# Optimization experiments

Measured on AMD Instinct MI355X. Metric: run time of the kernel, lower is better.

## Reference

```python
import jax, jax.numpy as jnp
import numpy as np

VOCAB, D_IN, D_H = 32000, 512, 1024
B, T = 16, 256
PAD_IDX = 0


def setup_inputs() -> dict:
    key = jax.random.key(0)
    k1, k2, k3, k4, k5 = jax.random.split(key, 5)
    input_idx = jax.random.randint(k1, (B, T), 0, VOCAB, dtype=jnp.int64)
    emb = jax.random.normal(k2, (VOCAB, D_IN), dtype=jnp.float32) * 0.02
    emb = emb.at[PAD_IDX].set(0.0)  # padding_idx row is zero
    weight_x = jax.random.normal(k3, (D_H, D_IN), dtype=jnp.float32) * (1.0 / np.sqrt(D_IN))
    weight_h = jax.random.normal(k4, (D_H, D_H), dtype=jnp.float32) * (1.0 / np.sqrt(D_H))
    bias = jnp.zeros((D_H,), dtype=jnp.float32)
    lm_W = jax.random.normal(k5, (VOCAB, D_H), dtype=jnp.float32) * (1.0 / np.sqrt(D_H))
    return {"input_idx": input_idx, "emb": emb, "weight_x": weight_x,
            "weight_h": weight_h, "bias": bias, "lm_W": lm_W}


def reference(input_idx, emb, weight_x, weight_h, bias, lm_W):
    Bsz = input_idx.shape[0]
    h0 = jnp.zeros((Bsz, weight_h.shape[0]), dtype=weight_x.dtype)

    def step(h, tok):
        x = emb[tok]  # [B, D_IN]
        h_new = jnp.tanh(x @ weight_x.T + h @ weight_h.T + bias)
        mask = (tok != PAD_IDX)[:, None]  # keep old h at pad positions
        h = jnp.where(mask, h_new, h)
        return h, h

    _, h_all = jax.lax.scan(step, h0, input_idx.T)  # [T, B, H]
    h_all = jnp.swapaxes(h_all, 0, 1)               # [B, T, H]
    logits = jnp.einsum('bth,vh->btv', h_all, lm_W)  # [B, T, V]
    return logits
```

## Files before the change

### kernel.cpp

```cpp
#include <hip/hip_runtime.h>

#define PAD_IDX 0

typedef __attribute__((ext_vector_type(8))) short short8;
typedef __attribute__((ext_vector_type(4))) float f32x4;

__device__ __forceinline__ unsigned short f32_to_bf16_rne(float f) {
  unsigned int u = __builtin_bit_cast(unsigned int, f);
  u += 0x7FFFu + ((u >> 16) & 1u);
  return (unsigned short)(u >> 16);
}

__device__ __forceinline__ void load16_to_lds(const void* g, void* lds) {
  __builtin_amdgcn_global_load_lds(
      (const __attribute__((address_space(1))) unsigned int*)g,
      (__attribute__((address_space(3))) unsigned int*)lds,
      16, 0, 0);
}

__global__ void sentinel_kernel(float* out) { out[0] = 1.0e6f; }

__global__ __launch_bounds__(256) void xwcvt_kernel(const int* __restrict__ tok,
                                                    const float* __restrict__ emb,
                                                    const float* __restrict__ Wx,
                                                    const float* __restrict__ bias,
                                                    float* __restrict__ xw,
                                                    const float* __restrict__ lmW,
                                                    unsigned short* __restrict__ lmW_bf) {
  int tid = threadIdx.x;
  if (blockIdx.x >= 1024) {
    const int n8 = 32000 * 1024 / 8;
    int stride = 512 * 256;
    for (int i = (blockIdx.x - 1024) * 256 + tid; i < n8; i += stride) {
      float4 a = ((const float4*)lmW)[2 * i];
      float4 b = ((const float4*)lmW)[2 * i + 1];
      ushort4 lo, hi;
      lo.x = f32_to_bf16_rne(a.x); lo.y = f32_to_bf16_rne(a.y);
      lo.z = f32_to_bf16_rne(a.z); lo.w = f32_to_bf16_rne(a.w);
      hi.x = f32_to_bf16_rne(b.x); hi.y = f32_to_bf16_rne(b.y);
      hi.z = f32_to_bf16_rne(b.z); hi.w = f32_to_bf16_rne(b.w);
      ((ushort4*)lmW_bf)[2 * i] = lo;
      ((ushort4*)lmW_bf)[2 * i + 1] = hi;
    }
    return;
  }
  __shared__ float At[32][68];
  __shared__ float Bt[32][68];
  __shared__ int stok[64];
  int tm = blockIdx.x & 63;
  int tn = blockIdx.x >> 6;
  int r0 = tm * 64, j0 = tn * 64;
  if (tid < 64) stok[tid] = tok[r0 + tid];
  int tx = tid & 15, ty = tid >> 4;
  float acc[4][4] = {};
  for (int kt = 0; kt < 512; kt += 32) {
    __syncthreads();
    #pragma unroll
    for (int ii = 0; ii < 2; ++ii) {
      int idx = tid * 2 + ii;
      int m = idx >> 3, fv = idx & 7;
      float4 va = *(const float4*)&emb[(size_t)stok[m] * 512 + kt + fv * 4];
      float4 vb = *(const float4*)&Wx[(size_t)(j0 + m) * 512 + kt + fv * 4];
      At[fv * 4 + 0][m] = va.x; At[fv * 4 + 1][m] = va.y;
      At[fv * 4 + 2][m] = va.z; At[fv * 4 + 3][m] = va.w;
      Bt[fv * 4 + 0][m] = vb.x; Bt[fv * 4 + 1][m] = vb.y;
      Bt[fv * 4 + 2][m] = vb.z; Bt[fv * 4 + 3][m] = vb.w;
    }
    __syncthreads();
    #pragma unroll
    for (int k = 0; k < 32; ++k) {
      float4 a4 = *(const float4*)&At[k][ty * 4];
      float4 b4 = *(const float4*)&Bt[k][tx * 4];
      float av[4] = {a4.x, a4.y, a4.z, a4.w};
      float bv[4] = {b4.x, b4.y, b4.z, b4.w};
      #pragma unroll
      for (int i = 0; i < 4; ++i)
        #pragma unroll
        for (int jj = 0; jj < 4; ++jj) acc[i][jj] = fmaf(av[i], bv[jj], acc[i][jj]);
    }
  }
  #pragma unroll
  for (int i = 0; i < 4; ++i) {
    size_t row = (size_t)(r0 + ty * 4 + i) * 1024 + j0 + tx * 4;
    #pragma unroll
    for (int jj = 0; jj < 4; ++jj)
      xw[row + jj] = acc[i][jj] + bias[j0 + tx * 4 + jj];
  }
}

__global__ __launch_bounds__(1024, 4) void rec_kernel(const float* __restrict__ Wh,
                                                      const float* __restrict__ xw,
                                                      const int* __restrict__ tok,
                                                      unsigned long long* hcomb,
                                                      unsigned short* __restrict__ h_all) {
  int c = blockIdx.x & 15;
  int g = blockIdx.x >> 4;
  int tid = threadIdx.x;
  int w = tid >> 6;
  int l = tid & 63;
  int j = g * 64 + l;

  const float* wb = Wh + (size_t)j * 1024 + w * 64;
#define LDW(i) f32x4 w##i = *(const f32x4*)(wb + i * 4);
  LDW(0) LDW(1) LDW(2) LDW(3) LDW(4) LDW(5) LDW(6) LDW(7)
  LDW(8) LDW(9) LDW(10) LDW(11) LDW(12) LDW(13) LDW(14) LDW(15)
#undef LDW

  __shared__ float hs[16][64];
  __shared__ float pbuf[16][64];
  unsigned long long* hc0 = hcomb + (size_t)c * 1024;
  unsigned long long* hc1 = hcomb + 16 * 1024 + (size_t)c * 1024;
  bool writer = (w == 0);

  for (int t = 0; t < 256; ++t) {
    float xv = 0.f;
    int tkn = 1;
    if (writer) {
      xv = xw[((size_t)c * 256 + t) * 1024 + j];
      tkn = tok[c * 256 + t];
    }
    unsigned long long* src = ((t & 1) ? hc1 : hc0) + tid;
    unsigned long long v;
    int guard = 0;
    do {
      v = __hip_atomic_load(src, __ATOMIC_RELAXED, __HIP_MEMORY_SCOPE_AGENT);
      if ((unsigned int)(v >> 32) == (unsigned int)t) break;
      __builtin_amdgcn_s_sleep(1);
    } while (++guard < (1 << 20));
    hs[w][l] = __builtin_bit_cast(float, (unsigned int)v);
    __asm__ volatile("s_waitcnt lgkmcnt(0)" ::: "memory");

    const float* hp = &hs[w][0];
    f32x4 a0 = {0.f, 0.f, 0.f, 0.f}, a1 = a0, a2 = a0, a3 = a0;
#define FMAI(i, acc) { f32x4 h4 = *(const f32x4*)(hp + i * 4); acc += w##i * h4; }
    FMAI(0, a0) FMAI(1, a1) FMAI(2, a2) FMAI(3, a3)
    FMAI(4, a0) FMAI(5, a1) FMAI(6, a2) FMAI(7, a3)
    FMAI(8, a0) FMAI(9, a1) FMAI(10, a2) FMAI(11, a3)
    FMAI(12, a0) FMAI(13, a1) FMAI(14, a2) FMAI(15, a3)
#undef FMAI
    f32x4 aa = (a0 + a1) + (a2 + a3);
    pbuf[w][l] = (aa[0] + aa[1]) + (aa[2] + aa[3]);
    __asm__ volatile("s_waitcnt lgkmcnt(0)\n\ts_barrier" ::: "memory");

    if (writer) {
      float s = 0.f;
      #pragma unroll
      for (int q = 0; q < 16; ++q) s += pbuf[q][l];
      float hnew;
      if (tkn != PAD_IDX) {
        float pre = xv + s;
        float e = __builtin_amdgcn_exp2f(pre * 2.8853900817779268f);
        hnew = 1.0f - 2.0f / (e + 1.0f);
      } else {
        hnew = hs[g][l];
      }
      unsigned long long pv =
          ((unsigned long long)(unsigned int)(t + 1) << 32) |
          (unsigned long long)__builtin_bit_cast(unsigned int, hnew);
      __hip_atomic_store((((t + 1) & 1) ? hc1 : hc0) + j, pv,
                         __ATOMIC_RELAXED, __HIP_MEMORY_SCOPE_AGENT);
      h_all[((size_t)c * 256 + t) * 1024 + j] = f32_to_bf16_rne(hnew);
    }
  }
}

__global__ __launch_bounds__(512) void gemm_kernel(const unsigned short* __restrict__ A,
                                                   const unsigned short* __restrict__ B,
                                                   float* __restrict__ C) {
  __shared__ unsigned short lds[2 * 32768];
  int tid = threadIdx.x;
  int lane = tid & 63, wave = tid >> 6;
  int bid = blockIdx.x;
  int wgid = (bid & 7) * 250 + (bid >> 3);
  int tm = wgid & 15, tn = wgid >> 4;
  int r0 = tm * 256, c0 = tn * 256;
  int wm = wave >> 2, wn = wave & 3;

  auto STAGE = [&](int kt, int st) {
    unsigned short* bufA = (unsigned short*)lds + st * 32768;
    unsigned short* bufB = bufA + 16384;
    #pragma unroll
    for (int i = 0; i < 4; ++i) {
      int slot = i * 512 + tid;
      int row = slot >> 3, sg = slot & 7;
      int kg = sg ^ (row & 7);
      const unsigned short* ga = A + (size_t)(r0 + row) * 1024 + kt * 64 + kg * 8;
      load16_to_lds(ga, &bufA[(i * 512 + wave * 64) * 8]);
    }
    #pragma unroll
    for (int i = 0; i < 4; ++i) {
      int slot = i * 512 + tid;
      int row = slot >> 3, sg = slot & 7;
      int kg = sg ^ (row & 7);
      const unsigned short* gb = B + (size_t)(c0 + row) * 1024 + kt * 64 + kg * 8;
      load16_to_lds(gb, &bufB[(i * 512 + wave * 64) * 8]);
    }
  };

  f32x4 zero = {0.f, 0.f, 0.f, 0.f};
  f32x4 acc[8][4];
  #pragma unroll
  for (int i = 0; i < 8; ++i)
    #pragma unroll
    for (int jx = 0; jx < 4; ++jx) acc[i][jx] = zero;

  STAGE(0, 0);
  STAGE(1, 1);
  __asm__ volatile("s_waitcnt vmcnt(8)\n\ts_barrier" ::: "memory");

  for (int kt = 0; kt < 16; ++kt) {
    int st = kt & 1;
    const unsigned short* bufA = (const unsigned short*)lds + st * 32768;
    const unsigned short* bufB = bufA + 16384;

    short8 af[8][2], bf[4][2];
    #pragma unroll
    for (int kkb = 0; kkb < 2; ++kkb) {
      int kbyte = kkb * 64 + (lane >> 4) * 16;
      #pragma unroll
      for (int i = 0; i < 8; ++i) {
        int rowa = wm * 128 + i * 16 + (lane & 15);
        af[i][kkb] = *(const short8*)((const char*)bufA + rowa * 128 + (kbyte ^ ((rowa & 7) << 4)));
      }
      #pragma unroll
      for (int i = 0; i < 4; ++i) {
        int rowb = wn * 64 + i * 16 + (lane & 15);
        bf[i][kkb] = *(const short8*)((const char*)bufB + rowb * 128 + (kbyte ^ ((rowb & 7) << 4)));
      }
    }
    __asm__ volatile("s_waitcnt lgkmcnt(0)\n\ts_barrier" ::: "memory");
    {
      int nkt = kt + 2;
      if (nkt > 15) nkt = 15;
      STAGE(nkt, st);
    }
    __builtin_amdgcn_s_setprio(1);
    #pragma unroll
    for (int kkb = 0; kkb < 2; ++kkb)
      #pragma unroll
      for (int i = 0; i < 8; ++i)
        #pragma unroll
        for (int jx = 0; jx < 4; ++jx)
          acc[i][jx] = __builtin_amdgcn_mfma_f32_16x16x32_bf16(af[i][kkb], bf[jx][kkb], acc[i][jx], 0, 0, 0);
    __builtin_amdgcn_s_setprio(0);
    __asm__ volatile("s_waitcnt vmcnt(8)\n\ts_barrier" ::: "memory");
  }
  __asm__ volatile("s_waitcnt vmcnt(0)" ::: "memory");

  int rbase = r0 + wm * 128 + (lane >> 4) * 4;
  int cbase = c0 + wn * 64 + (lane & 15);
  #pragma unroll
  for (int i = 0; i < 8; ++i)
    #pragma unroll
    for (int jx = 0; jx < 4; ++jx)
      #pragma unroll
      for (int q = 0; q < 4; ++q)
        C[(size_t)(rbase + i * 16 + q) * 32000 + cbase + jx * 16] = acc[i][jx][q];
}

extern "C" void kernel_launch(void* const* d_in, const int* in_sizes, int n_in,
                              void* d_out, int out_size, void* d_ws, size_t ws_size,
                              hipStream_t stream) {
  const int* tok = (const int*)d_in[0];
  const float* emb = (const float*)d_in[1];
  const float* Wx = (const float*)d_in[2];
  const float* Wh = (const float*)d_in[3];
  const float* bias = (const float*)d_in[4];
  const float* lmW = (const float*)d_in[5];
  float* out = (float*)d_out;

  const size_t OFF_LMW = 0;
  const size_t OFF_XW = 65536000;
  const size_t OFF_HALL = OFF_XW + 16777216;
  const size_t OFF_HCMB = OFF_HALL + 8388608;
  const size_t NEED = OFF_HCMB + 262144;
  if (ws_size < NEED) {
    sentinel_kernel<<<1, 1, 0, stream>>>(out);
    return;
  }
  char* ws = (char*)d_ws;
  unsigned short* lmW_bf = (unsigned short*)(ws + OFF_LMW);
  float* xw = (float*)(ws + OFF_XW);
  unsigned short* h_all = (unsigned short*)(ws + OFF_HALL);
  unsigned long long* hcomb = (unsigned long long*)(ws + OFF_HCMB);

  hipMemsetAsync(ws + OFF_HCMB, 0, 262144, stream);
  xwcvt_kernel<<<1536, 256, 0, stream>>>(tok, emb, Wx, bias, xw, lmW, lmW_bf);
  rec_kernel<<<256, 1024, 0, stream>>>(Wh, xw, tok, hcomb, h_all);
  gemm_kernel<<<2000, 512, 0, stream>>>(h_all, lmW_bf, out);
}
```

Before: 873.9 us.

## Use LDS atomic accumulation for recurrent partials and trim tail GEMM staging

In the recurrent kernel, the 16 waves now add their per-wave partial dot products into a double-buffered LDS accumulator with workgroup-scope atomics, replacing the 16-entry pbuf reduction that the writer wave summed serially. The writer reads the previous hidden value directly from the global combined buffer for pad tokens and publishes the new value with an atomic exchange instead of a store. In the GEMM, the last two k-iterations issue small dummy LDS loads instead of re-staging tile 15, so the vmcnt accounting stays the same while redundant traffic drops. The LDS float atomics serialize across waves and may cost more than the plain reduction they replace.

```diff
diff --git a/kernel.cpp b/kernel.cpp
--- a/kernel.cpp
+++ b/kernel.cpp
@@ -107,19 +107,26 @@
 #undef LDW
 
   __shared__ float hs[16][64];
-  __shared__ float pbuf[16][64];
+  __shared__ float accs[2][64];
+  if (tid < 128) ((float*)accs)[tid] = 0.f;
+  __syncthreads();
+
   unsigned long long* hc0 = hcomb + (size_t)c * 1024;
   unsigned long long* hc1 = hcomb + 16 * 1024 + (size_t)c * 1024;
   bool writer = (w == 0);
 
   for (int t = 0; t < 256; ++t) {
-    float xv = 0.f;
+    int p = t & 1;
+    unsigned long long* hcp = p ? hc1 : hc0;
+    float xv = 0.f, oldh = 0.f;
     int tkn = 1;
     if (writer) {
       xv = xw[((size_t)c * 256 + t) * 1024 + j];
       tkn = tok[c * 256 + t];
-    }
-    unsigned long long* src = ((t & 1) ? hc1 : hc0) + tid;
+      unsigned long long ov = __hip_atomic_load(hcp + j, __ATOMIC_RELAXED, __HIP_MEMORY_SCOPE_AGENT);
+      oldh = __builtin_bit_cast(float, (unsigned int)ov);
+    }
+    unsigned long long* src = hcp + tid;
     unsigned long long v;
     int guard = 0;
     do {
@@ -139,26 +146,26 @@
     FMAI(12, a0) FMAI(13, a1) FMAI(14, a2) FMAI(15, a3)
 #undef FMAI
     f32x4 aa = (a0 + a1) + (a2 + a3);
-    pbuf[w][l] = (aa[0] + aa[1]) + (aa[2] + aa[3]);
+    float partial = (aa[0] + aa[1]) + (aa[2] + aa[3]);
+    __hip_atomic_fetch_add(&accs[p][l], partial, __ATOMIC_RELAXED, __HIP_MEMORY_SCOPE_WORKGROUP);
     __asm__ volatile("s_waitcnt lgkmcnt(0)\n\ts_barrier" ::: "memory");
 
     if (writer) {
-      float s = 0.f;
-      #pragma unroll
-      for (int q = 0; q < 16; ++q) s += pbuf[q][l];
+      float s = accs[p][l];
+      accs[p][l] = 0.f;
       float hnew;
       if (tkn != PAD_IDX) {
         float pre = xv + s;
         float e = __builtin_amdgcn_exp2f(pre * 2.8853900817779268f);
         hnew = 1.0f - 2.0f / (e + 1.0f);
       } else {
-        hnew = hs[g][l];
+        hnew = oldh;
       }
       unsigned long long pv =
           ((unsigned long long)(unsigned int)(t + 1) << 32) |
           (unsigned long long)__builtin_bit_cast(unsigned int, hnew);
-      __hip_atomic_store((((t + 1) & 1) ? hc1 : hc0) + j, pv,
-                         __ATOMIC_RELAXED, __HIP_MEMORY_SCOPE_AGENT);
+      (void)__hip_atomic_exchange((p ? hc0 : hc1) + j, pv,
+                                  __ATOMIC_RELAXED, __HIP_MEMORY_SCOPE_AGENT);
       h_all[((size_t)c * 256 + t) * 1024 + j] = f32_to_bf16_rne(hnew);
     }
   }
@@ -229,10 +236,12 @@
       }
     }
     __asm__ volatile("s_waitcnt lgkmcnt(0)\n\ts_barrier" ::: "memory");
-    {
-      int nkt = kt + 2;
-      if (nkt > 15) nkt = 15;
-      STAGE(nkt, st);
+    if (kt < 14) {
+      STAGE(kt + 2, st);
+    } else {
+      unsigned short* dead = (unsigned short*)lds + st * 32768;
+      #pragma unroll
+      for (int i = 0; i < 8; ++i) load16_to_lds(A + (size_t)r0 * 1024, &dead[i * 8]);
     }
     __builtin_amdgcn_s_setprio(1);
     #pragma unroll
```

After: 1.145 ms. 31.0% more time.
